# Kernel optimization log

Measured on AMD Instinct MI355X. Metric: run time of the kernel, lower is better.

The kernel has to match this reference:

```python
import math
import jax, jax.numpy as jnp
import numpy as np

# MLA (absorb mode) constants from ModelArgs defaults
NOPE, ROPE, KVR, VH, H = 128, 64, 512, 128, 16
# YaRN-style scale: max_seq_len(16384) > original_seq_len(4096)
_MSCALE = 0.1 * 1.0 * math.log(40.0) + 1.0
SOFTMAX_SCALE = (NOPE + ROPE) ** -0.5 * _MSCALE * _MSCALE


def _apply_rope(x, cos, sin):
    # x: [b, s, h, r] with adjacent-pair complex layout; cos/sin: [s, r//2]
    b, s, h, r = x.shape
    xr = x.reshape(b, s, h, r // 2, 2)
    x0, x1 = xr[..., 0], xr[..., 1]
    c = cos[None, :, None, :]
    sn = sin[None, :, None, :]
    y0 = x0 * c - x1 * sn
    y1 = x0 * sn + x1 * c
    return jnp.stack([y0, y1], axis=-1).reshape(b, s, h, r)


def _rmsnorm(x, w, eps=1e-6):
    rms = jnp.sqrt(jnp.mean(x * x, axis=-1, keepdims=True) + eps)
    return x / rms * w


def setup_inputs() -> dict:
    key = jax.random.key(0)
    ks = jax.random.split(key, 6)
    B, S, D = 2, 2048, 2048
    x = jax.random.normal(ks[0], (B, S, D), dtype=jnp.float32)
    wq_w = jax.random.normal(ks[1], (H * (NOPE + ROPE), D), dtype=jnp.float32) * 0.02
    wkv_a_w = jax.random.normal(ks[2], (KVR + ROPE, D), dtype=jnp.float32) * 0.02
    kv_norm_w = jnp.ones((KVR,), dtype=jnp.float32)
    wkv_b_w = jax.random.normal(ks[3], (H * (NOPE + VH), KVR), dtype=jnp.float32) * 0.02
    wo_w = jax.random.normal(ks[4], (D, H * VH), dtype=jnp.float32) * 0.02
    # rotary angles: pos * inv_freq, theta=10000
    inv_freq = 1.0 / (10000.0 ** (np.arange(0, ROPE, 2, dtype=np.float32) / ROPE))
    angles = np.arange(S, dtype=np.float32)[:, None] * inv_freq[None, :]
    freqs = jnp.asarray(angles, dtype=jnp.float32)  # [S, 32]
    # causal additive mask [S, S]: 0 on/below diag, -inf above
    mask = jnp.triu(jnp.full((S, S), -jnp.inf, dtype=jnp.float32), k=1)
    return {"x": x, "wq_w": wq_w, "wkv_a_w": wkv_a_w, "kv_norm_w": kv_norm_w,
            "wkv_b_w": wkv_b_w, "wo_w": wo_w, "freqs": freqs, "mask": mask,
            "start_pos": 0}


def reference(x, wq_w, wkv_a_w, kv_norm_w, wkv_b_w, wo_w, freqs, mask, start_pos):
    # prefill: start_pos == 0, cache slice == freshly written KV
    b, s, d = x.shape
    cos, sin = jnp.cos(freqs), jnp.sin(freqs)

    q = jnp.einsum('bsd,od->bso', x, wq_w).reshape(b, s, H, NOPE + ROPE)
    q_nope, q_pe = q[..., :NOPE], q[..., NOPE:]
    q_pe = _apply_rope(q_pe, cos, sin)  # [b,s,H,ROPE]

    kv_full = jnp.einsum('bsd,od->bso', x, wkv_a_w)
    kv, k_pe = kv_full[..., :KVR], kv_full[..., KVR:]
    k_pe = _apply_rope(k_pe[:, :, None, :], cos, sin)[:, :, 0]  # [b,s,ROPE]
    kv_n = _rmsnorm(kv, kv_norm_w)  # [b,s,KVR] == kv_cache[:, :end_pos]

    wkv_b = wkv_b_w.reshape(H, NOPE + VH, KVR)
    # absorb: project q_nope into latent space
    q_abs = jnp.einsum('bshd,hdc->bshc', q_nope, wkv_b[:, :NOPE])
    scores = (jnp.einsum('bshc,btc->bsht', q_abs, kv_n)
              + jnp.einsum('bshr,btr->bsht', q_pe, k_pe)) * SOFTMAX_SCALE
    scores = scores + mask[:, None, :]  # broadcast over b, h
    p = jax.nn.softmax(scores.astype(jnp.float32), axis=-1).astype(x.dtype)

    out = jnp.einsum('bsht,btc->bshc', p, kv_n)
    out = jnp.einsum('bshc,hdc->bshd', out, wkv_b[:, -VH:])
    out = jnp.einsum('bsv,dv->bsd', out.reshape(b, s, H * VH), wo_w)
    return out
```

## Files before the change

### kernel.cpp

```cpp
#include <hip/hip_runtime.h>
#include <hip/hip_bf16.h>
#include <cmath>

typedef __bf16 bf16x8 __attribute__((ext_vector_type(8)));
typedef unsigned short u16x8_t __attribute__((ext_vector_type(8)));
typedef float f32x4 __attribute__((ext_vector_type(4)));
typedef unsigned short u16;

__device__ inline bf16x8 ld16(const void* p) {
  return __builtin_bit_cast(bf16x8, *reinterpret_cast<const u16x8_t*>(p));
}
__device__ inline void async16(const void* g, void* l) {
  __builtin_amdgcn_global_load_lds(
      (const __attribute__((address_space(1))) unsigned int*)g,
      (__attribute__((address_space(3))) unsigned int*)l, 16, 0, 0);
}
__device__ inline u16 f2bf(float v) {
  return __builtin_bit_cast(u16, __float2bfloat16(v));
}
__device__ inline float bf2f(u16 v) {
  unsigned int u = ((unsigned int)v) << 16;
  return __builtin_bit_cast(float, u);
}

__global__ void cast4(const float* __restrict__ src, u16* __restrict__ dst,
                      long n, long nsrc) {
  for (long i = (long)blockIdx.x * 256 + threadIdx.x; i * 4 < n;
       i += (long)gridDim.x * 256) {
    float4 v;
    if (i * 4 < nsrc) v = ((const float4*)src)[i];
    else { v.x = v.y = v.z = v.w = 0.f; }
    ushort4 o;
    o.x = f2bf(v.x); o.y = f2bf(v.y); o.z = f2bf(v.z); o.w = f2bf(v.w);
    ((ushort4*)dst)[i] = o;
  }
}

__global__ void fill_dbg(float* __restrict__ out, long n, float v) {
  for (long i = (long)blockIdx.x * 256 + threadIdx.x; i < n;
       i += (long)gridDim.x * 256) out[i] = v;
}

__global__ void prep_wkvb(const float* __restrict__ in, u16* __restrict__ outT,
                          u16* __restrict__ outV) {
  int h = blockIdx.x >> 7, d = blockIdx.x & 127;
  const float* r0 = in + (long)(h * 256 + d) * 512;
  const float* r1 = in + (long)(h * 256 + 128 + d) * 512;
  for (int c = threadIdx.x; c < 512; c += 256) {
    outT[((long)h * 512 + c) * 128 + d] = f2bf(r0[c]);
    outV[((long)h * 128 + d) * 512 + c] = f2bf(r1[c]);
  }
}

template <bool OUT_BF16>
__global__ __launch_bounds__(256) void gemm_bt(
    const u16* __restrict__ A, long lda,
    const u16* __restrict__ B, long ldb,
    void* __restrict__ Cv, long ldc, int K) {
  const long m0 = (long)blockIdx.y * 128, n0 = (long)blockIdx.x * 128;
  __shared__ __align__(16) u16 As[128][32];
  __shared__ __align__(16) u16 Bs[128][32];
  const int tid = threadIdx.x, lane = tid & 63, wv = tid >> 6;
  const int wm = (wv >> 1) * 64, wn = (wv & 1) * 64;
  const int lr = lane & 15, lg = lane >> 4;
  f32x4 acc[4][4];
#pragma unroll
  for (int i = 0; i < 4; i++)
#pragma unroll
    for (int j = 0; j < 4; j++) acc[i][j] = f32x4{0.f, 0.f, 0.f, 0.f};
  const int rr = tid >> 2, ko = (tid & 3) * 8;
  for (int k0 = 0; k0 < K; k0 += 32) {
    __syncthreads();
    async16(A + (m0 + rr) * lda + k0 + ko, &As[rr][ko]);
    async16(A + (m0 + rr + 64) * lda + k0 + ko, &As[rr + 64][ko]);
    async16(B + (n0 + rr) * ldb + k0 + ko, &Bs[rr][ko]);
    async16(B + (n0 + rr + 64) * ldb + k0 + ko, &Bs[rr + 64][ko]);
    __syncthreads();
    bf16x8 af[4], bfr[4];
#pragma unroll
    for (int mi = 0; mi < 4; mi++) af[mi] = ld16(&As[wm + mi * 16 + lr][lg * 8]);
#pragma unroll
    for (int ni = 0; ni < 4; ni++) bfr[ni] = ld16(&Bs[wn + ni * 16 + lr][lg * 8]);
#pragma unroll
    for (int mi = 0; mi < 4; mi++)
#pragma unroll
      for (int ni = 0; ni < 4; ni++)
        acc[mi][ni] = __builtin_amdgcn_mfma_f32_16x16x32_bf16(
            af[mi], bfr[ni], acc[mi][ni], 0, 0, 0);
  }
#pragma unroll
  for (int mi = 0; mi < 4; mi++)
#pragma unroll
    for (int ni = 0; ni < 4; ni++)
#pragma unroll
      for (int j = 0; j < 4; j++) {
        long row = m0 + wm + mi * 16 + lg * 4 + j;
        long col = n0 + wn + ni * 16 + lr;
        long idx = row * ldc + col;
        if (OUT_BF16) ((u16*)Cv)[idx] = f2bf(acc[mi][ni][j]);
        else ((float*)Cv)[idx] = acc[mi][ni][j];
      }
}

__global__ void fixup_q(const u16* __restrict__ q, const float* __restrict__ freqs,
                        u16* __restrict__ qn, u16* __restrict__ qpe) {
  long row = blockIdx.x;
  int s = (int)(row & 2047);
  const u16* qr = q + row * 3072;
  for (int j = threadIdx.x; j < 2048; j += 256) {
    int h = j >> 7, d = j & 127;
    qn[row * 2048 + j] = qr[h * 192 + d];
  }
  for (int j = threadIdx.x; j < 1024; j += 256) {
    int h = j >> 6, t = j & 63, p = t >> 1;
    float ang = freqs[s * 32 + p];
    float co = cosf(ang), sn = sinf(ang);
    float x0 = bf2f(qr[h * 192 + 128 + 2 * p]);
    float x1 = bf2f(qr[h * 192 + 128 + 2 * p + 1]);
    float y = (t & 1) ? (x0 * sn + x1 * co) : (x0 * co - x1 * sn);
    qpe[row * 1024 + j] = f2bf(y);
  }
}

__global__ void fixup_kv(const float* __restrict__ kvf, const float* __restrict__ w,
                         const float* __restrict__ freqs, u16* __restrict__ kvn,
                         u16* __restrict__ kpe) {
  long row = blockIdx.x;
  int s = (int)(row & 2047);
  const float* src = kvf + row * 640;
  int t = threadIdx.x;
  float x0 = src[t], x1 = src[t + 256];
  float ss = x0 * x0 + x1 * x1;
  for (int d = 1; d < 64; d <<= 1) ss += __shfl_xor(ss, d);
  __shared__ float wsum[4];
  if ((t & 63) == 0) wsum[t >> 6] = ss;
  __syncthreads();
  float tot = wsum[0] + wsum[1] + wsum[2] + wsum[3];
  float inv = rsqrtf(tot * (1.0f / 512.0f) + 1e-6f);
  kvn[row * 512 + t] = f2bf(x0 * inv * w[t]);
  kvn[row * 512 + t + 256] = f2bf(x1 * inv * w[t + 256]);
  if (t < 64) {
    int p = t >> 1;
    float ang = freqs[s * 32 + p];
    float co = cosf(ang), sn = sinf(ang);
    float a0 = src[512 + 2 * p], a1 = src[512 + 2 * p + 1];
    float y = (t & 1) ? (a0 * sn + a1 * co) : (a0 * co - a1 * sn);
    kpe[row * 64 + t] = f2bf(y);
  }
}

__global__ void transpose_kv(const u16* __restrict__ kvn, u16* __restrict__ kvt) {
  __shared__ u16 T[32][33];
  int b = blockIdx.z;
  int s0 = blockIdx.x * 32, c0 = blockIdx.y * 32;
  int r = threadIdx.x >> 5, c = threadIdx.x & 31;
  for (int rr = r; rr < 32; rr += 8)
    T[rr][c] = kvn[((long)b * 2048 + s0 + rr) * 512 + c0 + c];
  __syncthreads();
  for (int rr = r; rr < 32; rr += 8)
    kvt[((long)b * 512 + c0 + rr) * 2048 + s0 + c] = T[c][rr];
}

__device__ inline int swz(int row, int col) {
  return row * 512 + ((((col >> 3) ^ (row & 7)) << 3) | (col & 7));
}

__global__ __launch_bounds__(512, 2) void mla_flash(
    const u16* __restrict__ qn, const u16* __restrict__ qpe,
    const u16* __restrict__ wbT, const u16* __restrict__ wbV,
    const u16* __restrict__ kvn, const u16* __restrict__ kpe,
    const u16* __restrict__ kvt, u16* __restrict__ ov, float scale) {
  __shared__ __align__(16) u16 Ks[64][576];
  __shared__ __align__(16) u16 Vts[512][64];
  __shared__ __align__(16) u16 Psh[32][64];
  __shared__ float Msh[32][4];
  __shared__ float Lsh[32][4];
  u16* KQ = &Ks[0][0];
  u16* Pp = &Psh[0][0];

  const int qb = (63 - blockIdx.x) * 32;
  const int h = blockIdx.y, b = blockIdx.z;
  const int tid = threadIdx.x, lane = tid & 63, wv = tid >> 6;
  const int qg = wv >> 2, cg = wv & 3;
  const int lr = lane & 15, lg = lane >> 4;
  const long rowA = (long)b * 2048 + qb + qg * 16 + lr;
  const int rloc = qg * 16 + lg * 4;
  const int qrowD = qb + rloc;

  {
    f32x4 qacc[8];
#pragma unroll
    for (int i = 0; i < 8; i++) qacc[i] = f32x4{0.f, 0.f, 0.f, 0.f};
#pragma unroll
    for (int ks = 0; ks < 4; ks++) {
      bf16x8 aq = ld16(qn + rowA * 2048 + h * 128 + ks * 32 + lg * 8);
#pragma unroll
      for (int ni = 0; ni < 8; ni++) {
        bf16x8 bw = ld16(wbT + ((long)h * 512 + cg * 128 + ni * 16 + lr) * 128 +
                         ks * 32 + lg * 8);
        qacc[ni] = __builtin_amdgcn_mfma_f32_16x16x32_bf16(aq, bw, qacc[ni], 0, 0, 0);
      }
    }
#pragma unroll
    for (int ni = 0; ni < 8; ni++)
#pragma unroll
      for (int j = 0; j < 4; j++)
        KQ[swz(rloc + j, cg * 128 + ni * 16 + lr)] = f2bf(qacc[ni][j]);
  }
  __syncthreads();

  bf16x8 qf[18];
#pragma unroll
  for (int f = 0; f < 16; f++)
    qf[f] = ld16(&KQ[swz(qg * 16 + lr, f * 32 + lg * 8)]);
  {
    const u16* qp = qpe + rowA * 1024 + h * 64 + lg * 8;
    qf[16] = ld16(qp);
    qf[17] = ld16(qp + 32);
  }

  f32x4 O[8];
#pragma unroll
  for (int i = 0; i < 8; i++) O[i] = f32x4{0.f, 0.f, 0.f, 0.f};
  float mrow[4], lrow[4];
#pragma unroll
  for (int j = 0; j < 4; j++) { mrow[j] = -INFINITY; lrow[j] = 0.f; }

  const int nt = qb / 64 + 1;
  for (int t = 0; t < nt; t++) {
    const int tb = t * 64;
    __syncthreads();
    for (int c = tid; c < 4608; c += 512) {
      int r = c / 72, o = c - r * 72;
      int og = o ^ (r & 7);
      long grow = (long)b * 2048 + tb + r;
      const u16* src = (og < 64) ? (kvn + grow * 512 + og * 8)
                                 : (kpe + grow * 64 + (og - 64) * 8);
      async16(src, ((char*)Ks) + (long)c * 16);
    }
    for (int c = tid; c < 4096; c += 512) {
      int r = c >> 3, o = c & 7;
      int og = o ^ (r & 7);
      const u16* src = kvt + ((long)b * 512 + r) * 2048 + tb + og * 8;
      async16(src, ((char*)Vts) + (long)c * 16);
    }
    __syncthreads();

    f32x4 sc = f32x4{0.f, 0.f, 0.f, 0.f};
    {
      const char* kbase = ((const char*)Ks) + (cg * 16 + lr) * 1152;
      const int sx = lr & 7;
#pragma unroll
      for (int f = 0; f < 18; f++) {
        bf16x8 kf = ld16(kbase + (((f * 4 + lg) ^ sx) * 16));
        sc = __builtin_amdgcn_mfma_f32_16x16x32_bf16(qf[f], kf, sc, 0, 0, 0);
      }
    }
    float s4[4], mt[4];
    const int colg = tb + cg * 16 + lr;
#pragma unroll
    for (int j = 0; j < 4; j++) {
      s4[j] = (colg <= qrowD + j) ? sc[j] * scale : -INFINITY;
      mt[j] = s4[j];
    }
#pragma unroll
    for (int d = 1; d < 16; d <<= 1)
#pragma unroll
      for (int j = 0; j < 4; j++) mt[j] = fmaxf(mt[j], __shfl_xor(mt[j], d));
    if (lr == 0)
#pragma unroll
      for (int j = 0; j < 4; j++) Msh[rloc + j][cg] = mt[j];
    __syncthreads();

    float fac[4], p4[4], ls[4];
#pragma unroll
    for (int j = 0; j < 4; j++) {
      float4 m4 = *(const float4*)Msh[rloc + j];
      float mn = fmaxf(fmaxf(fmaxf(m4.x, m4.y), fmaxf(m4.z, m4.w)), mrow[j]);
      fac[j] = __expf(mrow[j] - mn);
      mrow[j] = mn;
      p4[j] = __expf(s4[j] - mn);
      ls[j] = p4[j];
    }
#pragma unroll
    for (int d = 1; d < 16; d <<= 1)
#pragma unroll
      for (int j = 0; j < 4; j++) ls[j] += __shfl_xor(ls[j], d);
    if (lr == 0)
#pragma unroll
      for (int j = 0; j < 4; j++) Lsh[rloc + j][cg] = ls[j];
#pragma unroll
    for (int j = 0; j < 4; j++) {
      int row = rloc + j;
      int chunk = (cg * 2 + (lr >> 3)) ^ (row & 7);
      Pp[row * 64 + chunk * 8 + (lr & 7)] = f2bf(p4[j]);
#pragma unroll
      for (int ni = 0; ni < 8; ni++) O[ni][j] *= fac[j];
    }
    __syncthreads();

#pragma unroll
    for (int j = 0; j < 4; j++) {
      float4 l4 = *(const float4*)Lsh[rloc + j];
      lrow[j] = lrow[j] * fac[j] + (l4.x + l4.y + l4.z + l4.w);
    }
    bf16x8 pf[2];
#pragma unroll
    for (int ks = 0; ks < 2; ks++)
      pf[ks] = ld16(&Pp[(qg * 16 + lr) * 64 + (((ks * 4 + lg) ^ (lr & 7)) * 8)]);
    const char* vbase = (const char*)Vts;
#pragma unroll
    for (int ks = 0; ks < 2; ks++)
#pragma unroll
      for (int ni = 0; ni < 8; ni++) {
        int row = cg * 128 + ni * 16 + lr;
        bf16x8 vf = ld16(vbase + row * 128 + (((ks * 4 + lg) ^ (lr & 7)) * 16));
        O[ni] = __builtin_amdgcn_mfma_f32_16x16x32_bf16(pf[ks], vf, O[ni], 0, 0, 0);
      }
  }

  __syncthreads();
  float inv4[4];
#pragma unroll
  for (int j = 0; j < 4; j++) inv4[j] = 1.0f / lrow[j];
#pragma unroll
  for (int ni = 0; ni < 8; ni++)
#pragma unroll
    for (int j = 0; j < 4; j++)
      KQ[swz(rloc + j, cg * 128 + ni * 16 + lr)] = f2bf(O[ni][j] * inv4[j]);
  __syncthreads();
  f32x4 vacc[2];
  vacc[0] = f32x4{0.f, 0.f, 0.f, 0.f};
  vacc[1] = f32x4{0.f, 0.f, 0.f, 0.f};
#pragma unroll
  for (int ks = 0; ks < 16; ks++) {
    bf16x8 ao = ld16(&KQ[swz(qg * 16 + lr, ks * 32 + lg * 8)]);
#pragma unroll
    for (int ni = 0; ni < 2; ni++) {
      bf16x8 bw = ld16(wbV + ((long)h * 128 + cg * 32 + ni * 16 + lr) * 512 +
                       ks * 32 + lg * 8);
      vacc[ni] = __builtin_amdgcn_mfma_f32_16x16x32_bf16(ao, bw, vacc[ni], 0, 0, 0);
    }
  }
#pragma unroll
  for (int ni = 0; ni < 2; ni++)
#pragma unroll
    for (int j = 0; j < 4; j++)
      ov[((long)b * 2048 + qrowD + j) * 2048 + h * 128 + cg * 32 + ni * 16 + lr] =
          f2bf(vacc[ni][j]);
}

extern "C" void kernel_launch(void* const* d_in, const int* in_sizes, int n_in,
                              void* d_out, int out_size, void* d_ws, size_t ws_size,
                              hipStream_t stream) {
  const float* x     = (const float*)d_in[0];
  const float* wq    = (const float*)d_in[1];
  const float* wkva  = (const float*)d_in[2];
  const float* knw   = (const float*)d_in[3];
  const float* wkvb  = (const float*)d_in[4];
  const float* wo    = (const float*)d_in[5];
  const float* freqs = (const float*)d_in[6];
  float* out = (float*)d_out;

  char* ws = (char*)d_ws;
  size_t off = 0;
  auto alloc = [&](size_t bytes) {
    char* p = ws + off;
    off += (bytes + 255) & ~(size_t)255;
    return p;
  };
  u16* qn    = (u16*)alloc(8388608ull * 2);
  u16* xb    = (u16*)alloc(8388608ull * 2);
  u16* wqb   = (u16*)alloc(6291456ull * 2);
  u16* wkvab = (u16*)alloc(1310720ull * 2);
  float* kvf = (float*)alloc(2621440ull * 4);
  u16* wbT   = (u16*)alloc(1048576ull * 2);
  u16* wbV   = (u16*)alloc(1048576ull * 2);
  u16* wob   = (u16*)alloc(4194304ull * 2);
  u16* qpe_  = (u16*)alloc(4194304ull * 2);
  u16* kvn   = (u16*)alloc(2097152ull * 2);
  u16* kpe   = (u16*)alloc(262144ull * 2);
  u16* kvt   = (u16*)alloc(2097152ull * 2);
  u16* ovb   = (u16*)alloc(8388608ull * 2);
  u16* qbig = (u16*)d_out;

  if (off > ws_size) {
    fill_dbg<<<2048, 256, 0, stream>>>(out, 8388608L, (float)(ws_size >> 20));
    return;
  }

  double msc = 0.1 * log(40.0) + 1.0;
  float scale = (float)(pow(192.0, -0.5) * msc * msc);

  cast4<<<1024, 256, 0, stream>>>(x, xb, 8388608L, 8388608L);
  cast4<<<1024, 256, 0, stream>>>(wq, wqb, 6291456L, 6291456L);
  cast4<<<1024, 256, 0, stream>>>(wkva, wkvab, 1310720L, 1179648L);
  cast4<<<1024, 256, 0, stream>>>(wo, wob, 4194304L, 4194304L);
  prep_wkvb<<<2048, 256, 0, stream>>>(wkvb, wbT, wbV);

  gemm_bt<true><<<dim3(24, 32, 1), 256, 0, stream>>>(
      xb, 2048, wqb, 2048, qbig, 3072, 2048);
  gemm_bt<false><<<dim3(5, 32, 1), 256, 0, stream>>>(
      xb, 2048, wkvab, 2048, kvf, 640, 2048);

  fixup_q<<<4096, 256, 0, stream>>>(qbig, freqs, qn, qpe_);
  fixup_kv<<<4096, 256, 0, stream>>>(kvf, knw, freqs, kvn, kpe);
  transpose_kv<<<dim3(64, 16, 2), 256, 0, stream>>>(kvn, kvt);

  mla_flash<<<dim3(64, 16, 2), 512, 0, stream>>>(qn, qpe_, wbT, wbV, kvn, kpe,
                                                 kvt, ovb, scale);

  gemm_bt<false><<<dim3(16, 32, 1), 256, 0, stream>>>(
      ovb, 2048, wob, 2048, out, 2048, 2048);
}
```

Before: 1.166 ms.

## Restructure MLA flash kernel with 64-row query tiles and double-buffered K

The flash attention kernel now handles 64 query rows per block instead of 32 and walks key tiles of 32 rows. Absorbed Q is kept in shared memory and K is double-buffered so the next tile loads asynchronously while the current one is computed. V fragments and k_pe are read directly from global memory into registers rather than staged through LDS, and the running max moves into a shared ping-pong array. Full syncthreads are replaced with custom waitcnt+barrier helpers; the goal is more reuse of K/V per block and overlap of loads with compute, at the cost of more registers, more LDS and a more intricate synchronisation scheme.

```diff
diff --git a/kernel.cpp b/kernel.cpp
--- a/kernel.cpp
+++ b/kernel.cpp
@@ -21,6 +21,16 @@
 __device__ inline float bf2f(u16 v) {
   unsigned int u = ((unsigned int)v) << 16;
   return __builtin_bit_cast(float, u);
+}
+__device__ inline void bar_lds() {
+  asm volatile("s_waitcnt lgkmcnt(0)" ::: "memory");
+  __builtin_amdgcn_sched_barrier(0);
+  __builtin_amdgcn_s_barrier();
+}
+__device__ inline void bar_all() {
+  asm volatile("s_waitcnt vmcnt(0) lgkmcnt(0)" ::: "memory");
+  __builtin_amdgcn_sched_barrier(0);
+  __builtin_amdgcn_s_barrier();
 }
 
 __global__ void cast4(const float* __restrict__ src, u16* __restrict__ dst,
@@ -161,7 +171,7 @@
     kvt[((long)b * 512 + c0 + rr) * 2048 + s0 + c] = T[c][rr];
 }
 
-__device__ inline int swz(int row, int col) {
+__device__ inline int qswz(int row, int col) {
   return row * 512 + ((((col >> 3) ^ (row & 7)) << 3) | (col & 7));
 }
 
@@ -170,97 +180,113 @@
     const u16* __restrict__ wbT, const u16* __restrict__ wbV,
     const u16* __restrict__ kvn, const u16* __restrict__ kpe,
     const u16* __restrict__ kvt, u16* __restrict__ ov, float scale) {
-  __shared__ __align__(16) u16 Ks[64][576];
-  __shared__ __align__(16) u16 Vts[512][64];
-  __shared__ __align__(16) u16 Psh[32][64];
-  __shared__ float Msh[32][4];
-  __shared__ float Lsh[32][4];
-  u16* KQ = &Ks[0][0];
-  u16* Pp = &Psh[0][0];
-
-  const int qb = (63 - blockIdx.x) * 32;
+  __shared__ __align__(16) u16 Qs[64 * 512];
+  __shared__ __align__(16) u16 Ks[2][32 * 512];
+  __shared__ __align__(16) u16 Psh[64 * 32];
+  __shared__ float Msh[64][2];
+  __shared__ float Lsh[64][2];
+  __shared__ float Mrun[2][64];
+
+  const int qb = (31 - (int)blockIdx.x) * 64;
   const int h = blockIdx.y, b = blockIdx.z;
   const int tid = threadIdx.x, lane = tid & 63, wv = tid >> 6;
-  const int qg = wv >> 2, cg = wv & 3;
   const int lr = lane & 15, lg = lane >> 4;
-  const long rowA = (long)b * 2048 + qb + qg * 16 + lr;
-  const int rloc = qg * 16 + lg * 4;
-  const int qrowD = qb + rloc;
-
+  const int rg = wv & 3, cp = wv >> 2;
+  const int qg = wv & 1, cg = wv >> 1;
+  const int rloc = rg * 16 + lg * 4;
+
+  if (tid < 64) Mrun[0][tid] = -INFINITY;
   {
-    f32x4 qacc[8];
-#pragma unroll
-    for (int i = 0; i < 8; i++) qacc[i] = f32x4{0.f, 0.f, 0.f, 0.f};
-#pragma unroll
-    for (int ks = 0; ks < 4; ks++) {
-      bf16x8 aq = ld16(qn + rowA * 2048 + h * 128 + ks * 32 + lg * 8);
-#pragma unroll
-      for (int ni = 0; ni < 8; ni++) {
-        bf16x8 bw = ld16(wbT + ((long)h * 512 + cg * 128 + ni * 16 + lr) * 128 +
+    const int pr = rg, pc = cp;
+    const u16* aqp =
+        qn + ((long)b * 2048 + qb + pr * 16 + lr) * 2048 + h * 128 + lg * 8;
+    bf16x8 aq[4];
+#pragma unroll
+    for (int ks = 0; ks < 4; ks++) aq[ks] = ld16(aqp + ks * 32);
+#pragma unroll
+    for (int ni = 0; ni < 16; ni++) {
+      f32x4 acc = f32x4{0.f, 0.f, 0.f, 0.f};
+#pragma unroll
+      for (int ks = 0; ks < 4; ks++) {
+        bf16x8 bw = ld16(wbT + ((long)h * 512 + pc * 256 + ni * 16 + lr) * 128 +
                          ks * 32 + lg * 8);
-        qacc[ni] = __builtin_amdgcn_mfma_f32_16x16x32_bf16(aq, bw, qacc[ni], 0, 0, 0);
-      }
-    }
+        acc = __builtin_amdgcn_mfma_f32_16x16x32_bf16(aq[ks], bw, acc, 0, 0, 0);
+      }
+#pragma unroll
+      for (int j = 0; j < 4; j++)
+        Qs[qswz(pr * 16 + lg * 4 + j, pc * 256 + ni * 16 + lr)] = f2bf(acc[j]);
+    }
+  }
+  bf16x8 qpf0, qpf1;
+  {
+    const u16* qpp =
+        qpe + ((long)b * 2048 + qb + rg * 16 + lr) * 1024 + h * 64 + lg * 8;
+    qpf0 = ld16(qpp);
+    qpf1 = ld16(qpp + 32);
+  }
+
+  f32x4 O[2][8];
+  float lrow[2][4];
+#pragma unroll
+  for (int rb = 0; rb < 2; rb++) {
+#pragma unroll
+    for (int ni = 0; ni < 8; ni++) O[rb][ni] = f32x4{0.f, 0.f, 0.f, 0.f};
+#pragma unroll
+    for (int j = 0; j < 4; j++) lrow[rb][j] = 0.f;
+  }
+
+  auto stageK = [&](int t, int buf) {
+    const int tb = t * 32;
+#pragma unroll
+    for (int it = 0; it < 4; it++) {
+      int c = tid + it * 512;
+      int r = c >> 6, o = c & 63;
+      int og = o ^ (r & 7);
+      const u16* src = kvn + ((long)b * 2048 + tb + r) * 512 + og * 8;
+      async16(src, ((char*)Ks[buf]) + (long)c * 16);
+    }
+  };
+
+  stageK(0, 0);
+  bar_all();
+
+  const int nt = qb / 32 + 2;
+  for (int t = 0; t < nt; t++) {
+    const int cur = t & 1;
+    const int tb = t * 32;
+    if (t + 1 < nt) stageK(t + 1, cur ^ 1);
+    bf16x8 vf[8];
 #pragma unroll
     for (int ni = 0; ni < 8; ni++)
-#pragma unroll
-      for (int j = 0; j < 4; j++)
-        KQ[swz(rloc + j, cg * 128 + ni * 16 + lr)] = f2bf(qacc[ni][j]);
-  }
-  __syncthreads();
-
-  bf16x8 qf[18];
-#pragma unroll
-  for (int f = 0; f < 16; f++)
-    qf[f] = ld16(&KQ[swz(qg * 16 + lr, f * 32 + lg * 8)]);
-  {
-    const u16* qp = qpe + rowA * 1024 + h * 64 + lg * 8;
-    qf[16] = ld16(qp);
-    qf[17] = ld16(qp + 32);
-  }
-
-  f32x4 O[8];
-#pragma unroll
-  for (int i = 0; i < 8; i++) O[i] = f32x4{0.f, 0.f, 0.f, 0.f};
-  float mrow[4], lrow[4];
-#pragma unroll
-  for (int j = 0; j < 4; j++) { mrow[j] = -INFINITY; lrow[j] = 0.f; }
-
-  const int nt = qb / 64 + 1;
-  for (int t = 0; t < nt; t++) {
-    const int tb = t * 64;
-    __syncthreads();
-    for (int c = tid; c < 4608; c += 512) {
-      int r = c / 72, o = c - r * 72;
-      int og = o ^ (r & 7);
-      long grow = (long)b * 2048 + tb + r;
-      const u16* src = (og < 64) ? (kvn + grow * 512 + og * 8)
-                                 : (kpe + grow * 64 + (og - 64) * 8);
-      async16(src, ((char*)Ks) + (long)c * 16);
-    }
-    for (int c = tid; c < 4096; c += 512) {
-      int r = c >> 3, o = c & 7;
-      int og = o ^ (r & 7);
-      const u16* src = kvt + ((long)b * 512 + r) * 2048 + tb + og * 8;
-      async16(src, ((char*)Vts) + (long)c * 16);
-    }
-    __syncthreads();
-
-    f32x4 sc = f32x4{0.f, 0.f, 0.f, 0.f};
+      vf[ni] = ld16(kvt + ((long)b * 512 + cg * 128 + ni * 16 + lr) * 2048 + tb +
+                    lg * 8);
+    const u16* kpp = kpe + ((long)b * 2048 + tb + cp * 16 + lr) * 64 + lg * 8;
+    bf16x8 kp0 = ld16(kpp), kp1 = ld16(kpp + 32);
+
+    f32x4 a0 = f32x4{0.f, 0.f, 0.f, 0.f}, a1 = f32x4{0.f, 0.f, 0.f, 0.f};
     {
-      const char* kbase = ((const char*)Ks) + (cg * 16 + lr) * 1152;
-      const int sx = lr & 7;
-#pragma unroll
-      for (int f = 0; f < 18; f++) {
-        bf16x8 kf = ld16(kbase + (((f * 4 + lg) ^ sx) * 16));
-        sc = __builtin_amdgcn_mfma_f32_16x16x32_bf16(qf[f], kf, sc, 0, 0, 0);
-      }
+      const int qrow = rg * 16 + lr, krow = cp * 16 + lr;
+      const u16* kb = Ks[cur];
+#pragma unroll
+      for (int f = 0; f < 8; f++) {
+        bf16x8 q0 = ld16(&Qs[qswz(qrow, (2 * f) * 32 + lg * 8)]);
+        bf16x8 k0 = ld16(&kb[krow * 512 +
+                             ((((2 * f) * 4 + lg) ^ (krow & 7)) << 3)]);
+        a0 = __builtin_amdgcn_mfma_f32_16x16x32_bf16(q0, k0, a0, 0, 0, 0);
+        bf16x8 q1 = ld16(&Qs[qswz(qrow, (2 * f + 1) * 32 + lg * 8)]);
+        bf16x8 k1 = ld16(&kb[krow * 512 +
+                             ((((2 * f + 1) * 4 + lg) ^ (krow & 7)) << 3)]);
+        a1 = __builtin_amdgcn_mfma_f32_16x16x32_bf16(q1, k1, a1, 0, 0, 0);
+      }
+      a0 = __builtin_amdgcn_mfma_f32_16x16x32_bf16(qpf0, kp0, a0, 0, 0, 0);
+      a1 = __builtin_amdgcn_mfma_f32_16x16x32_bf16(qpf1, kp1, a1, 0, 0, 0);
     }
     float s4[4], mt[4];
-    const int colg = tb + cg * 16 + lr;
 #pragma unroll
     for (int j = 0; j < 4; j++) {
-      s4[j] = (colg <= qrowD + j) ? sc[j] * scale : -INFINITY;
+      int grow = qb + rloc + j, col = tb + cp * 16 + lr;
+      float sv = (a0[j] + a1[j]) * scale;
+      s4[j] = (col <= grow) ? sv : -INFINITY;
       mt[j] = s4[j];
     }
 #pragma unroll
@@ -269,16 +295,15 @@
       for (int j = 0; j < 4; j++) mt[j] = fmaxf(mt[j], __shfl_xor(mt[j], d));
     if (lr == 0)
 #pragma unroll
-      for (int j = 0; j < 4; j++) Msh[rloc + j][cg] = mt[j];
-    __syncthreads();
-
-    float fac[4], p4[4], ls[4];
+      for (int j = 0; j < 4; j++) Msh[rloc + j][cp] = mt[j];
+    bar_lds();
+
+    float p4[4], ls[4], mnS[4];
 #pragma unroll
     for (int j = 0; j < 4; j++) {
-      float4 m4 = *(const float4*)Msh[rloc + j];
-      float mn = fmaxf(fmaxf(fmaxf(m4.x, m4.y), fmaxf(m4.z, m4.w)), mrow[j]);
-      fac[j] = __expf(mrow[j] - mn);
-      mrow[j] = mn;
+      int row = rloc + j;
+      float mn = fmaxf(fmaxf(Msh[row][0], Msh[row][1]), Mrun[cur][row]);
+      mnS[j] = mn;
       p4[j] = __expf(s4[j] - mn);
       ls[j] = p4[j];
     }
@@ -288,66 +313,91 @@
       for (int j = 0; j < 4; j++) ls[j] += __shfl_xor(ls[j], d);
     if (lr == 0)
 #pragma unroll
-      for (int j = 0; j < 4; j++) Lsh[rloc + j][cg] = ls[j];
+      for (int j = 0; j < 4; j++) Lsh[rloc + j][cp] = ls[j];
+    if (cp == 0 && lr == 0)
+#pragma unroll
+      for (int j = 0; j < 4; j++) Mrun[cur ^ 1][rloc + j] = mnS[j];
 #pragma unroll
     for (int j = 0; j < 4; j++) {
       int row = rloc + j;
-      int chunk = (cg * 2 + (lr >> 3)) ^ (row & 7);
-      Pp[row * 64 + chunk * 8 + (lr & 7)] = f2bf(p4[j]);
-#pragma unroll
-      for (int ni = 0; ni < 8; ni++) O[ni][j] *= fac[j];
-    }
-    __syncthreads();
-
-#pragma unroll
-    for (int j = 0; j < 4; j++) {
-      float4 l4 = *(const float4*)Lsh[rloc + j];
-      lrow[j] = lrow[j] * fac[j] + (l4.x + l4.y + l4.z + l4.w);
-    }
+      int cx = ((cp * 2 + (lr >> 3)) ^ (row & 3));
+      Psh[row * 32 + (cx << 3) + (lr & 7)] = f2bf(p4[j]);
+    }
+    float fac[2][4];
+#pragma unroll
+    for (int rb = 0; rb < 2; rb++)
+#pragma unroll
+      for (int j = 0; j < 4; j++) {
+        int row = qg * 32 + rb * 16 + lg * 4 + j;
+        float mp = Mrun[cur][row];
+        float mn = fmaxf(fmaxf(Msh[row][0], Msh[row][1]), mp);
+        fac[rb][j] = __expf(mp - mn);
+      }
+#pragma unroll
+    for (int rb = 0; rb < 2; rb++)
+#pragma unroll
+      for (int ni = 0; ni < 8; ni++)
+#pragma unroll
+        for (int j = 0; j < 4; j++) O[rb][ni][j] *= fac[rb][j];
+    bar_lds();
+
+#pragma unroll
+    for (int rb = 0; rb < 2; rb++)
+#pragma unroll
+      for (int j = 0; j < 4; j++) {
+        int row = qg * 32 + rb * 16 + lg * 4 + j;
+        lrow[rb][j] = lrow[rb][j] * fac[rb][j] + Lsh[row][0] + Lsh[row][1];
+      }
     bf16x8 pf[2];
 #pragma unroll
-    for (int ks = 0; ks < 2; ks++)
-      pf[ks] = ld16(&Pp[(qg * 16 + lr) * 64 + (((ks * 4 + lg) ^ (lr & 7)) * 8)]);
-    const char* vbase = (const char*)Vts;
-#pragma unroll
-    for (int ks = 0; ks < 2; ks++)
-#pragma unroll
-      for (int ni = 0; ni < 8; ni++) {
-        int row = cg * 128 + ni * 16 + lr;
-        bf16x8 vf = ld16(vbase + row * 128 + (((ks * 4 + lg) ^ (lr & 7)) * 16));
-        O[ni] = __builtin_amdgcn_mfma_f32_16x16x32_bf16(pf[ks], vf, O[ni], 0, 0, 0);
-      }
-  }
-
-  __syncthreads();
-  float inv4[4];
-#pragma unroll
-  for (int j = 0; j < 4; j++) inv4[j] = 1.0f / lrow[j];
-#pragma unroll
-  for (int ni = 0; ni < 8; ni++)
-#pragma unroll
-    for (int j = 0; j < 4; j++)
-      KQ[swz(rloc + j, cg * 128 + ni * 16 + lr)] = f2bf(O[ni][j] * inv4[j]);
-  __syncthreads();
-  f32x4 vacc[2];
-  vacc[0] = f32x4{0.f, 0.f, 0.f, 0.f};
-  vacc[1] = f32x4{0.f, 0.f, 0.f, 0.f};
-#pragma unroll
-  for (int ks = 0; ks < 16; ks++) {
-    bf16x8 ao = ld16(&KQ[swz(qg * 16 + lr, ks * 32 + lg * 8)]);
-#pragma unroll
-    for (int ni = 0; ni < 2; ni++) {
-      bf16x8 bw = ld16(wbV + ((long)h * 128 + cg * 32 + ni * 16 + lr) * 512 +
-                       ks * 32 + lg * 8);
-      vacc[ni] = __builtin_amdgcn_mfma_f32_16x16x32_bf16(ao, bw, vacc[ni], 0, 0, 0);
-    }
-  }
-#pragma unroll
-  for (int ni = 0; ni < 2; ni++)
-#pragma unroll
-    for (int j = 0; j < 4; j++)
-      ov[((long)b * 2048 + qrowD + j) * 2048 + h * 128 + cg * 32 + ni * 16 + lr] =
-          f2bf(vacc[ni][j]);
+    for (int rb = 0; rb < 2; rb++) {
+      int prow = qg * 32 + rb * 16 + lr;
+      pf[rb] = ld16(&Psh[prow * 32 + ((lg ^ (prow & 3)) << 3)]);
+    }
+#pragma unroll
+    for (int rb = 0; rb < 2; rb++)
+#pragma unroll
+      for (int ni = 0; ni < 8; ni++)
+        O[rb][ni] =
+            __builtin_amdgcn_mfma_f32_16x16x32_bf16(pf[rb], vf[ni], O[rb][ni], 0, 0, 0);
+    bar_all();
+  }
+
+#pragma unroll
+  for (int rb = 0; rb < 2; rb++) {
+    float inv[4];
+#pragma unroll
+    for (int j = 0; j < 4; j++) inv[j] = 1.0f / lrow[rb][j];
+#pragma unroll
+    for (int ni = 0; ni < 8; ni++)
+#pragma unroll
+      for (int j = 0; j < 4; j++)
+        Qs[qswz(qg * 32 + rb * 16 + lg * 4 + j, cg * 128 + ni * 16 + lr)] =
+            f2bf(O[rb][ni][j] * inv[j]);
+  }
+  bar_lds();
+  {
+    const int er = rg, ec = cp;
+    f32x4 vacc[4];
+#pragma unroll
+    for (int ni = 0; ni < 4; ni++) vacc[ni] = f32x4{0.f, 0.f, 0.f, 0.f};
+#pragma unroll
+    for (int ks = 0; ks < 16; ks++) {
+      bf16x8 ao = ld16(&Qs[qswz(er * 16 + lr, ks * 32 + lg * 8)]);
+#pragma unroll
+      for (int ni = 0; ni < 4; ni++) {
+        bf16x8 bw = ld16(wbV + ((long)h * 128 + ec * 64 + ni * 16 + lr) * 512 +
+                         ks * 32 + lg * 8);
+        vacc[ni] = __builtin_amdgcn_mfma_f32_16x16x32_bf16(ao, bw, vacc[ni], 0, 0, 0);
+      }
+    }
+#pragma unroll
+    for (int ni = 0; ni < 4; ni++)
+#pragma unroll
+      for (int j = 0; j < 4; j++)
+        ov[((long)b * 2048 + qb + er * 16 + lg * 4 + j) * 2048 + h * 128 +
+           ec * 64 + ni * 16 + lr] = f2bf(vacc[ni][j]);
+  }
 }
 
 extern "C" void kernel_launch(void* const* d_in, const int* in_sizes, int n_in,
@@ -407,7 +457,7 @@
   fixup_kv<<<4096, 256, 0, stream>>>(kvf, knw, freqs, kvn, kpe);
   transpose_kv<<<dim3(64, 16, 2), 256, 0, stream>>>(kvn, kvt);
 
-  mla_flash<<<dim3(64, 16, 2), 512, 0, stream>>>(qn, qpe_, wbT, wbV, kvn, kpe,
+  mla_flash<<<dim3(32, 16, 2), 512, 0, stream>>>(qn, qpe_, wbT, wbV, kvn, kpe,
                                                  kvt, ovb, scale);
 
   gemm_bt<false><<<dim3(16, 32, 1), 256, 0, stream>>>(
```

Measured after the change: 1.607 ms. 1.38x slower.

## Halve KV tile to 32 keys and raise occupancy target in MLA flash kernel

Applied to the files above, without the earlier changes.

Shrinks the per-iteration key tile from 64 to 32 columns, which roughly halves the LDS footprint for K, V-transposed and P buffers, and raises the launch bound to 4 blocks per CU. With only two 16-column score groups, waves whose cg index is 2 or 3 now duplicate the score computation, and only the non-duplicate waves write the max, sum and P values. The swizzles for V and P are reworked for the 32-wide rows. The intent is higher occupancy and better latency hiding, at the cost of redundant QK MFMAs, twice as many loop iterations and barriers, and tighter register limits that may cause spills.

```diff
diff --git a/kernel.cpp b/kernel.cpp
--- a/kernel.cpp
+++ b/kernel.cpp
@@ -165,27 +165,27 @@
   return row * 512 + ((((col >> 3) ^ (row & 7)) << 3) | (col & 7));
 }
 
-__global__ __launch_bounds__(512, 2) void mla_flash(
+__global__ __launch_bounds__(512, 4) void mla_flash(
     const u16* __restrict__ qn, const u16* __restrict__ qpe,
     const u16* __restrict__ wbT, const u16* __restrict__ wbV,
     const u16* __restrict__ kvn, const u16* __restrict__ kpe,
     const u16* __restrict__ kvt, u16* __restrict__ ov, float scale) {
-  __shared__ __align__(16) u16 Ks[64][576];
-  __shared__ __align__(16) u16 Vts[512][64];
-  __shared__ __align__(16) u16 Psh[32][64];
-  __shared__ float Msh[32][4];
-  __shared__ float Lsh[32][4];
+  __shared__ __align__(16) u16 Ks[32][576];
+  __shared__ __align__(16) u16 Vts[512][32];
+  __shared__ __align__(16) u16 Psh[32][32];
+  __shared__ float Msh[32][2];
+  __shared__ float Lsh[32][2];
   u16* KQ = &Ks[0][0];
-  u16* Pp = &Psh[0][0];
-
-  const int qb = (63 - blockIdx.x) * 32;
+
+  const int qb = (63 - (int)blockIdx.x) * 32;
   const int h = blockIdx.y, b = blockIdx.z;
   const int tid = threadIdx.x, lane = tid & 63, wv = tid >> 6;
+  const int lr = lane & 15, lg = lane >> 4;
   const int qg = wv >> 2, cg = wv & 3;
-  const int lr = lane & 15, lg = lane >> 4;
-  const long rowA = (long)b * 2048 + qb + qg * 16 + lr;
+  const int cp = wv & 1, dup = (wv >> 1) & 1;
   const int rloc = qg * 16 + lg * 4;
   const int qrowD = qb + rloc;
+  const long rowA = (long)b * 2048 + qb + qg * 16 + lr;
 
   {
     f32x4 qacc[8];
@@ -226,11 +226,11 @@
 #pragma unroll
   for (int j = 0; j < 4; j++) { mrow[j] = -INFINITY; lrow[j] = 0.f; }
 
-  const int nt = qb / 64 + 1;
+  const int nt = qb / 32 + 1;
   for (int t = 0; t < nt; t++) {
-    const int tb = t * 64;
-    __syncthreads();
-    for (int c = tid; c < 4608; c += 512) {
+    const int tb = t * 32;
+    __syncthreads();
+    for (int c = tid; c < 2304; c += 512) {
       int r = c / 72, o = c - r * 72;
       int og = o ^ (r & 7);
       long grow = (long)b * 2048 + tb + r;
@@ -238,17 +238,17 @@
                                  : (kpe + grow * 64 + (og - 64) * 8);
       async16(src, ((char*)Ks) + (long)c * 16);
     }
-    for (int c = tid; c < 4096; c += 512) {
-      int r = c >> 3, o = c & 7;
-      int og = o ^ (r & 7);
-      const u16* src = kvt + ((long)b * 512 + r) * 2048 + tb + og * 8;
+    for (int c = tid; c < 2048; c += 512) {
+      int r = c >> 2, p = c & 3;
+      int o = p ^ ((r >> 1) & 3);
+      const u16* src = kvt + ((long)b * 512 + r) * 2048 + tb + o * 8;
       async16(src, ((char*)Vts) + (long)c * 16);
     }
     __syncthreads();
 
     f32x4 sc = f32x4{0.f, 0.f, 0.f, 0.f};
     {
-      const char* kbase = ((const char*)Ks) + (cg * 16 + lr) * 1152;
+      const char* kbase = ((const char*)Ks) + (cp * 16 + lr) * 1152;
       const int sx = lr & 7;
 #pragma unroll
       for (int f = 0; f < 18; f++) {
@@ -257,7 +257,7 @@
       }
     }
     float s4[4], mt[4];
-    const int colg = tb + cg * 16 + lr;
+    const int colg = tb + cp * 16 + lr;
 #pragma unroll
     for (int j = 0; j < 4; j++) {
       s4[j] = (colg <= qrowD + j) ? sc[j] * scale : -INFINITY;
@@ -267,16 +267,16 @@
     for (int d = 1; d < 16; d <<= 1)
 #pragma unroll
       for (int j = 0; j < 4; j++) mt[j] = fmaxf(mt[j], __shfl_xor(mt[j], d));
-    if (lr == 0)
-#pragma unroll
-      for (int j = 0; j < 4; j++) Msh[rloc + j][cg] = mt[j];
+    if (dup == 0 && lr == 0)
+#pragma unroll
+      for (int j = 0; j < 4; j++) Msh[rloc + j][cp] = mt[j];
     __syncthreads();
 
     float fac[4], p4[4], ls[4];
 #pragma unroll
     for (int j = 0; j < 4; j++) {
-      float4 m4 = *(const float4*)Msh[rloc + j];
-      float mn = fmaxf(fmaxf(fmaxf(m4.x, m4.y), fmaxf(m4.z, m4.w)), mrow[j]);
+      int row = rloc + j;
+      float mn = fmaxf(fmaxf(Msh[row][0], Msh[row][1]), mrow[j]);
       fac[j] = __expf(mrow[j] - mn);
       mrow[j] = mn;
       p4[j] = __expf(s4[j] - mn);
@@ -286,37 +286,40 @@
     for (int d = 1; d < 16; d <<= 1)
 #pragma unroll
       for (int j = 0; j < 4; j++) ls[j] += __shfl_xor(ls[j], d);
-    if (lr == 0)
-#pragma unroll
-      for (int j = 0; j < 4; j++) Lsh[rloc + j][cg] = ls[j];
+    if (dup == 0) {
+      if (lr == 0)
+#pragma unroll
+        for (int j = 0; j < 4; j++) Lsh[rloc + j][cp] = ls[j];
+#pragma unroll
+      for (int j = 0; j < 4; j++) {
+        int row = rloc + j;
+        int c2 = (cp * 2 + (lr >> 3)) ^ ((row >> 1) & 3);
+        Psh[row][(c2 << 3) + (lr & 7)] = f2bf(p4[j]);
+      }
+    }
+#pragma unroll
+    for (int ni = 0; ni < 8; ni++)
+#pragma unroll
+      for (int j = 0; j < 4; j++) O[ni][j] *= fac[j];
+    __syncthreads();
+
 #pragma unroll
     for (int j = 0; j < 4; j++) {
       int row = rloc + j;
-      int chunk = (cg * 2 + (lr >> 3)) ^ (row & 7);
-      Pp[row * 64 + chunk * 8 + (lr & 7)] = f2bf(p4[j]);
-#pragma unroll
-      for (int ni = 0; ni < 8; ni++) O[ni][j] *= fac[j];
-    }
-    __syncthreads();
-
-#pragma unroll
-    for (int j = 0; j < 4; j++) {
-      float4 l4 = *(const float4*)Lsh[rloc + j];
-      lrow[j] = lrow[j] * fac[j] + (l4.x + l4.y + l4.z + l4.w);
-    }
-    bf16x8 pf[2];
-#pragma unroll
-    for (int ks = 0; ks < 2; ks++)
-      pf[ks] = ld16(&Pp[(qg * 16 + lr) * 64 + (((ks * 4 + lg) ^ (lr & 7)) * 8)]);
-    const char* vbase = (const char*)Vts;
-#pragma unroll
-    for (int ks = 0; ks < 2; ks++)
-#pragma unroll
-      for (int ni = 0; ni < 8; ni++) {
-        int row = cg * 128 + ni * 16 + lr;
-        bf16x8 vf = ld16(vbase + row * 128 + (((ks * 4 + lg) ^ (lr & 7)) * 16));
-        O[ni] = __builtin_amdgcn_mfma_f32_16x16x32_bf16(pf[ks], vf, O[ni], 0, 0, 0);
-      }
+      lrow[j] = lrow[j] * fac[j] + Lsh[row][0] + Lsh[row][1];
+    }
+    bf16x8 pf;
+    {
+      int prow = qg * 16 + lr;
+      pf = ld16(&Psh[prow][(lg ^ ((prow >> 1) & 3)) << 3]);
+    }
+#pragma unroll
+    for (int ni = 0; ni < 8; ni++) {
+      int vrow = cg * 128 + ni * 16 + lr;
+      bf16x8 vf = ld16(((const char*)Vts) + vrow * 64 +
+                       ((lg ^ ((vrow >> 1) & 3)) << 4));
+      O[ni] = __builtin_amdgcn_mfma_f32_16x16x32_bf16(pf, vf, O[ni], 0, 0, 0);
+    }
   }
 
   __syncthreads();
```

Result: slower. 2.245 ms (+92.5%).
